# Optimization experiments

Measured on AMD Instinct MI355X. Metric: run time of the kernel, lower is better.

Reference implementation:

```python
import jax, jax.numpy as jnp
import numpy as np

EMBED_DIM = 1024
N_HEADS = 16
HEAD_DIM = EMBED_DIM // N_HEADS


def setup_inputs() -> dict:
    key = jax.random.key(0)
    ks = jax.random.split(key, 11)
    B, S = 4, 2048
    s = 0.02
    return {
        "queries": jax.random.normal(ks[0], (B, S, EMBED_DIM), dtype=jnp.float32),
        "keys": jax.random.normal(ks[1], (B, S, EMBED_DIM), dtype=jnp.float32),
        "values": jax.random.normal(ks[2], (B, S, EMBED_DIM), dtype=jnp.float32),
        "W_q": jax.random.normal(ks[3], (HEAD_DIM, HEAD_DIM), dtype=jnp.float32) * s,
        "b_q": jax.random.normal(ks[4], (HEAD_DIM,), dtype=jnp.float32) * s,
        "W_k": jax.random.normal(ks[5], (HEAD_DIM, HEAD_DIM), dtype=jnp.float32) * s,
        "b_k": jax.random.normal(ks[6], (HEAD_DIM,), dtype=jnp.float32) * s,
        "W_v": jax.random.normal(ks[7], (HEAD_DIM, HEAD_DIM), dtype=jnp.float32) * s,
        "b_v": jax.random.normal(ks[8], (HEAD_DIM,), dtype=jnp.float32) * s,
        "W_p": jax.random.normal(ks[9], (EMBED_DIM, EMBED_DIM), dtype=jnp.float32) * s,
        "b_p": jax.random.normal(ks[10], (EMBED_DIM,), dtype=jnp.float32) * s,
    }


def reference(queries, keys, values, W_q, b_q, W_k, b_k, W_v, b_v, W_p, b_p):
    B, S, _ = queries.shape
    scale = HEAD_DIM ** 0.5  # module uses head_dim ** (1/2)
    # split heads: [B, S, H, hd]
    q = queries.reshape(B, S, N_HEADS, HEAD_DIM)
    k = keys.reshape(B, S, N_HEADS, HEAD_DIM)
    v = values.reshape(B, S, N_HEADS, HEAD_DIM)
    # per-head projections (weights shared across heads); torch Linear: x @ W.T + b
    q = jnp.einsum('bshd,ed->bhse', q, W_q) + b_q
    k = jnp.einsum('bshd,ed->bhse', k, W_k) + b_k
    v = jnp.einsum('bshd,ed->bhse', v, W_v) + b_v
    # scaled dot-product attention
    scores = jnp.einsum('bhqd,bhkd->bhqk', q, k) / scale  # [B,H,S,S]
    attn = jax.nn.softmax(scores, axis=-1)
    ctx = jnp.einsum('bhqk,bhkd->bhqd', attn, v)  # [B,H,S,hd]
    # merge heads and final projection
    ctx = ctx.transpose(0, 2, 1, 3).reshape(B, S, EMBED_DIM)
    return ctx @ W_p.T + b_p
```

## Files before the change

### kernel.cpp

```cpp
#include <hip/hip_runtime.h>
#include <hip/hip_bf16.h>

#define EMBED 1024
#define NH 16
#define HD 64
#define BSZ 4
#define SSZ 2048
#define LSTR 72

typedef __attribute__((ext_vector_type(8))) short short8;
typedef __attribute__((ext_vector_type(4))) short short4v;
typedef __attribute__((ext_vector_type(4))) float float4v;
typedef __attribute__((ext_vector_type(2))) unsigned int uint2v;

__device__ inline float4v mfma16(short8 a, short8 b, float4v c) {
    return __builtin_amdgcn_mfma_f32_16x16x32_bf16(a, b, c, 0, 0, 0);
}

__device__ inline float fexp2(float x) { return __builtin_amdgcn_exp2f(x); }

__device__ inline short f2bf(float f) {
    unsigned u = __builtin_bit_cast(unsigned, f);
    return (short)((u + 0x8000u) >> 16);
}
__device__ inline unsigned pk2(float a, float b) {
    unsigned ua = __builtin_bit_cast(unsigned, a);
    unsigned ub = __builtin_bit_cast(unsigned, b);
    return ((ua + 0x8000u) >> 16) | (((ub + 0x8000u) >> 16) << 16);
}
__device__ inline short8 ld8_f32_bf16(const float* p) {
    float4v lo = *(const float4v*)p;
    float4v hi = *(const float4v*)(p + 4);
    short8 r;
#pragma unroll
    for (int i = 0; i < 4; ++i) { r[i] = f2bf(lo[i]); r[i + 4] = f2bf(hi[i]); }
    return r;
}

__device__ inline void glds16(const short* gsrc, short* ldst) {
    __builtin_amdgcn_global_load_lds(
        (const __attribute__((address_space(1))) unsigned int*)gsrc,
        (__attribute__((address_space(3))) unsigned int*)ldst,
        16, 0, 0);
}

__global__ __launch_bounds__(256) void wp_cvt_kernel(
    const float* __restrict__ Wp, short* __restrict__ Wpb)
{
    int i = (blockIdx.x * 256 + threadIdx.x) * 4;
    float4v v = *(const float4v*)(Wp + i);
    short4v s;
#pragma unroll
    for (int j = 0; j < 4; ++j) s[j] = f2bf(v[j]);
    *(short4v*)(Wpb + i) = s;
}

__global__ __launch_bounds__(256) void qkv_kernel(
    const float* __restrict__ q_in, const float* __restrict__ k_in,
    const float* __restrict__ v_in,
    const float* __restrict__ Wq, const float* __restrict__ bq,
    const float* __restrict__ Wk, const float* __restrict__ bk,
    const float* __restrict__ Wv, const float* __restrict__ bv,
    short* __restrict__ qp, short* __restrict__ kp, short* __restrict__ vt)
{
    __shared__ __align__(16) short Xb[64 * LSTR];
    __shared__ __align__(16) short Wb[64 * LSTR];

    int z = blockIdx.z;
    const float* X    = z == 0 ? q_in : (z == 1 ? k_in : v_in);
    const float* W    = z == 0 ? Wq   : (z == 1 ? Wk   : Wv);
    const float* bias = z == 0 ? bq   : (z == 1 ? bk   : bv);
    const float scale = z == 0 ? 0.125f * 1.44269504f : 1.0f;

    int tid = threadIdx.x;
    int wave = tid >> 6, lane = tid & 63, quad = lane >> 4, l16 = lane & 15;
    int h = blockIdx.y;
    int rbase = blockIdx.x * 64;
    int b = rbase >> 11;
    int sbase = rbase & (SSZ - 1);
    int bh = b * NH + h;

    int srow = tid >> 2, c16 = (tid & 3) * 16;
    {
        const float* xsrc = X + (size_t)(rbase + srow) * EMBED + h * HD + c16;
        short8 x0 = ld8_f32_bf16(xsrc);
        short8 x1 = ld8_f32_bf16(xsrc + 8);
        *(short8*)&Xb[srow * LSTR + c16] = x0;
        *(short8*)&Xb[srow * LSTR + c16 + 8] = x1;
        const float* wsrc = W + (size_t)srow * HD + c16;
        short8 w0 = ld8_f32_bf16(wsrc);
        short8 w1 = ld8_f32_bf16(wsrc + 8);
        *(short8*)&Wb[srow * LSTR + c16] = w0;
        *(short8*)&Wb[srow * LSTR + c16 + 8] = w1;
    }
    __syncthreads();

    short8 a0 = *(const short8*)&Xb[(wave * 16 + l16) * LSTR + quad * 8];
    short8 a1 = *(const short8*)&Xb[(wave * 16 + l16) * LSTR + 32 + quad * 8];
    float4v acc[4];
#pragma unroll
    for (int nt = 0; nt < 4; ++nt) acc[nt] = (float4v)(0.f);
#pragma unroll
    for (int nt = 0; nt < 4; ++nt) {
        short8 b0 = *(const short8*)&Wb[(nt * 16 + l16) * LSTR + quad * 8];
        short8 b1 = *(const short8*)&Wb[(nt * 16 + l16) * LSTR + 32 + quad * 8];
        acc[nt] = mfma16(a0, b0, acc[nt]);
        acc[nt] = mfma16(a1, b1, acc[nt]);
    }
    __syncthreads();

    if (z < 2) {
#pragma unroll
        for (int nt = 0; nt < 4; ++nt) {
            float bv_ = bias[nt * 16 + l16];
#pragma unroll
            for (int r = 0; r < 4; ++r) {
                float val = (acc[nt][r] + bv_) * scale;
                Xb[(wave * 16 + quad * 4 + r) * LSTR + nt * 16 + l16] = f2bf(val);
            }
        }
        __syncthreads();
        short8 r0 = *(const short8*)&Xb[srow * LSTR + c16];
        short8 r1 = *(const short8*)&Xb[srow * LSTR + c16 + 8];
        short* Y = z == 0 ? qp : kp;
        size_t o = ((size_t)bh * SSZ + sbase + srow) * HD + c16;
        *(short8*)&Y[o] = r0;
        *(short8*)&Y[o + 8] = r1;
    } else {
#pragma unroll
        for (int nt = 0; nt < 4; ++nt) {
            float bv_ = bias[nt * 16 + l16];
            uint2v p;
            p[0] = pk2(acc[nt][0] + bv_, acc[nt][1] + bv_);
            p[1] = pk2(acc[nt][2] + bv_, acc[nt][3] + bv_);
            *(uint2v*)&Xb[(nt * 16 + l16) * LSTR + wave * 16 + quad * 4] = p;
        }
        __syncthreads();
        short8 r0 = *(const short8*)&Xb[srow * LSTR + c16];
        short8 r1 = *(const short8*)&Xb[srow * LSTR + c16 + 8];
        size_t o = ((size_t)bh * HD + srow) * SSZ + sbase + c16;
        *(short8*)&vt[o] = r0;
        *(short8*)&vt[o + 8] = r1;
    }
}

__global__ __launch_bounds__(512, 4) void attn_kernel(
    const short* __restrict__ qp, const short* __restrict__ kp,
    const short* __restrict__ vt, short* __restrict__ ctx)
{
    __shared__ __align__(16) short Kls[64 * LSTR];
    __shared__ __align__(16) short Vls[64 * LSTR];
    __shared__ __align__(16) short Pl[8 * 32 * LSTR];

    int tid = threadIdx.x;
    int wave = tid >> 6, lane = tid & 63, quad = lane >> 4, l16 = lane & 15;
    int bh = blockIdx.x;
    int b = bh >> 4, h = bh & 15;
    int qrow0 = blockIdx.y * 256 + wave * 32;

    const short* Qb = qp + (size_t)bh * SSZ * HD;
    const short* Kb = kp + (size_t)bh * SSZ * HD;
    const short* Vb = vt + (size_t)bh * HD * SSZ;

    int srow = tid >> 3;
    int scol = (tid & 7) * 8;
    const short* ksrc = Kb + srow * HD + scol;
    const short* vsrc = Vb + (size_t)srow * SSZ + scol;
    short* kdst = &Kls[srow * LSTR + scol];
    short* vdst = &Vls[srow * LSTR + scol];

    short8 qf[2][2];
#pragma unroll
    for (int nt = 0; nt < 2; ++nt)
#pragma unroll
        for (int c = 0; c < 2; ++c)
            qf[nt][c] = *(const short8*)&Qb[(size_t)(qrow0 + nt * 16 + l16) * HD + c * 32 + quad * 8];

    const short one = (short)0x3F80;
    short8 ones = {one, one, one, one, one, one, one, one};

    float4v oacc[4][2];
#pragma unroll
    for (int dt = 0; dt < 4; ++dt)
#pragma unroll
        for (int nt = 0; nt < 2; ++nt) oacc[dt][nt] = (float4v)(0.f);
    float4v lacc[2];
    lacc[0] = (float4v)(0.f); lacc[1] = (float4v)(0.f);

    short* Pw = Pl + wave * 32 * LSTR;

    {
        short8 kr = *(const short8*)(ksrc);
        short8 vr = *(const short8*)(vsrc);
        *(short8*)kdst = kr;
        *(short8*)vdst = vr;
    }
    __syncthreads();

    for (int kt = 0; kt < SSZ / 64; ++kt) {
        short8 krn, vrn;
        if (kt < 31) {
            krn = *(const short8*)(ksrc + (kt + 1) * 64 * HD);
            vrn = *(const short8*)(vsrc + (kt + 1) * 64);
        }
        float4v sacc[4][2];
#pragma unroll
        for (int mt = 0; mt < 4; ++mt) {
            sacc[mt][0] = (float4v)(0.f); sacc[mt][1] = (float4v)(0.f);
        }
#pragma unroll
        for (int mt = 0; mt < 4; ++mt)
#pragma unroll
            for (int c = 0; c < 2; ++c) {
                short8 kf = *(const short8*)&Kls[(mt * 16 + l16) * LSTR + c * 32 + quad * 8];
                sacc[mt][0] = mfma16(kf, qf[0][c], sacc[mt][0]);
                sacc[mt][1] = mfma16(kf, qf[1][c], sacc[mt][1]);
            }
#pragma unroll
        for (int mt = 0; mt < 4; ++mt)
#pragma unroll
            for (int nt = 0; nt < 2; ++nt) {
                float e0 = fexp2(sacc[mt][nt][0]);
                float e1 = fexp2(sacc[mt][nt][1]);
                float e2 = fexp2(sacc[mt][nt][2]);
                float e3 = fexp2(sacc[mt][nt][3]);
                uint2v p; p[0] = pk2(e0, e1); p[1] = pk2(e2, e3);
                *(uint2v*)&Pw[(nt * 16 + l16) * LSTR + mt * 16 + quad * 4] = p;
            }
        short8 pf[2][2];
#pragma unroll
        for (int nt = 0; nt < 2; ++nt)
#pragma unroll
            for (int c = 0; c < 2; ++c)
                pf[nt][c] = *(const short8*)&Pw[(nt * 16 + l16) * LSTR + c * 32 + quad * 8];
#pragma unroll
        for (int nt = 0; nt < 2; ++nt)
#pragma unroll
            for (int c = 0; c < 2; ++c)
                lacc[nt] = mfma16(ones, pf[nt][c], lacc[nt]);
#pragma unroll
        for (int dt = 0; dt < 4; ++dt)
#pragma unroll
            for (int c = 0; c < 2; ++c) {
                short8 vf = *(const short8*)&Vls[(dt * 16 + l16) * LSTR + c * 32 + quad * 8];
                oacc[dt][0] = mfma16(vf, pf[0][c], oacc[dt][0]);
                oacc[dt][1] = mfma16(vf, pf[1][c], oacc[dt][1]);
            }
        __syncthreads();
        if (kt < 31) {
            *(short8*)kdst = krn;
            *(short8*)vdst = vrn;
        }
        __syncthreads();
    }
    float rl[2];
    rl[0] = 1.0f / lacc[0][0];
    rl[1] = 1.0f / lacc[1][0];
#pragma unroll
    for (int dt = 0; dt < 4; ++dt)
#pragma unroll
        for (int nt = 0; nt < 2; ++nt) {
            uint2v p;
            p[0] = pk2(oacc[dt][nt][0] * rl[nt], oacc[dt][nt][1] * rl[nt]);
            p[1] = pk2(oacc[dt][nt][2] * rl[nt], oacc[dt][nt][3] * rl[nt]);
            size_t o = ((size_t)(b * SSZ + qrow0 + nt * 16 + l16)) * EMBED
                       + h * HD + dt * 16 + quad * 4;
            *(uint2v*)&ctx[o] = p;
        }
}

__global__ __launch_bounds__(256) void proj_kernel(
    const short* __restrict__ ctx, const short* __restrict__ Wpb,
    const float* __restrict__ bp, float* __restrict__ out)
{
    __shared__ __align__(16) short Als[128 * 64];
    __shared__ __align__(16) short Bls[128 * 64];

    int tid = threadIdx.x;
    int wave = tid >> 6, lane = tid & 63, quad = lane >> 4, l16 = lane & 15;
    int wm = wave >> 1, wn = wave & 1;
    int row0 = blockIdx.x * 128;
    int col0 = blockIdx.y * 128;

    int lrow = lane >> 3;
    int lcol = (lane & 7) * 8;
    const short* ag = ctx + (size_t)(row0 + wave * 32 + lrow) * EMBED + lcol;
    const short* bg = Wpb + (size_t)(col0 + wave * 32 + lrow) * EMBED + lcol;

    float4v acc[4][4];
#pragma unroll
    for (int mt = 0; mt < 4; ++mt)
#pragma unroll
        for (int nt = 0; nt < 4; ++nt) acc[mt][nt] = (float4v)(0.f);

    for (int kc = 0; kc < EMBED / 64; ++kc) {
#pragma unroll
        for (int i = 0; i < 4; ++i) {
            glds16(ag + (size_t)(i * 8) * EMBED + kc * 64,
                   &Als[(wave * 32 + i * 8) * 64]);
            glds16(bg + (size_t)(i * 8) * EMBED + kc * 64,
                   &Bls[(wave * 32 + i * 8) * 64]);
        }
        __syncthreads();
#pragma unroll
        for (int ks = 0; ks < 2; ++ks) {
            short8 af[4], bf[4];
#pragma unroll
            for (int mt = 0; mt < 4; ++mt)
                af[mt] = *(const short8*)&Als[(wm * 64 + mt * 16 + l16) * 64 + ks * 32 + quad * 8];
#pragma unroll
            for (int nt = 0; nt < 4; ++nt)
                bf[nt] = *(const short8*)&Bls[(wn * 64 + nt * 16 + l16) * 64 + ks * 32 + quad * 8];
#pragma unroll
            for (int mt = 0; mt < 4; ++mt)
#pragma unroll
                for (int nt = 0; nt < 4; ++nt)
                    acc[mt][nt] = mfma16(af[mt], bf[nt], acc[mt][nt]);
        }
        __syncthreads();
    }
#pragma unroll
    for (int nt = 0; nt < 4; ++nt) {
        float bias = bp[col0 + wn * 64 + nt * 16 + l16];
#pragma unroll
        for (int mt = 0; mt < 4; ++mt)
#pragma unroll
            for (int r = 0; r < 4; ++r) {
                int row = row0 + wm * 64 + mt * 16 + quad * 4 + r;
                out[(size_t)row * EMBED + col0 + wn * 64 + nt * 16 + l16] = acc[mt][nt][r] + bias;
            }
    }
}

extern "C" void kernel_launch(void* const* d_in, const int* in_sizes, int n_in,
                              void* d_out, int out_size, void* d_ws, size_t ws_size,
                              hipStream_t stream) {
    const float* q_in = (const float*)d_in[0];
    const float* k_in = (const float*)d_in[1];
    const float* v_in = (const float*)d_in[2];
    const float* Wq   = (const float*)d_in[3];
    const float* bq   = (const float*)d_in[4];
    const float* Wk   = (const float*)d_in[5];
    const float* bk   = (const float*)d_in[6];
    const float* Wv   = (const float*)d_in[7];
    const float* bv   = (const float*)d_in[8];
    const float* Wp   = (const float*)d_in[9];
    const float* bp   = (const float*)d_in[10];

    const size_t TENS = (size_t)BSZ * SSZ * EMBED;
    short* ws  = (short*)d_ws;
    short* qp  = ws;
    short* kp  = qp + TENS;
    short* vtp = kp + TENS;
    short* ctx = vtp + TENS;
    short* wpb = ctx + TENS;

    wp_cvt_kernel<<<dim3(EMBED * EMBED / 1024), 256, 0, stream>>>(Wp, wpb);
    qkv_kernel<<<dim3(BSZ * SSZ / 64, NH, 3), 256, 0, stream>>>(
        q_in, k_in, v_in, Wq, bq, Wk, bk, Wv, bv, qp, kp, vtp);
    attn_kernel<<<dim3(BSZ * NH, SSZ / 256), 512, 0, stream>>>(qp, kp, vtp, ctx);
    proj_kernel<<<dim3(BSZ * SSZ / 128, EMBED / 128), 256, 0, stream>>>(
        ctx, wpb, bp, (float*)d_out);
}
```

Measured before the change: 277.6 us.

## Restructure QKV projection: 16-row blocks over all heads, register-resident weights

The QKV projection kernel now gives each block 16 sequence rows and all 16 heads, with each wave handling 4 heads. Shared weight fragments are loaded once into registers and reused across heads, cutting the 3D grid to 2D and removing the LDS staging of X. For Q/K the MFMA operands are swapped so results are written straight to global memory. V goes through a small per-wave LDS buffer for the transpose, and the bf16 packing now uses a byte-permute intrinsic. The trade-off is smaller, less coalesced global writes, with more work and more registers per block.

Measured after the change: 282.7 us. About the same (+1.8%).

```diff
diff --git a/kernel.cpp b/kernel.cpp
--- a/kernel.cpp
+++ b/kernel.cpp
@@ -7,11 +7,12 @@
 #define BSZ 4
 #define SSZ 2048
 #define LSTR 72
+#define BSTR 24
 
 typedef __attribute__((ext_vector_type(8))) short short8;
-typedef __attribute__((ext_vector_type(4))) short short4v;
 typedef __attribute__((ext_vector_type(4))) float float4v;
 typedef __attribute__((ext_vector_type(2))) unsigned int uint2v;
+typedef __attribute__((ext_vector_type(4))) unsigned int uint4v;
 
 __device__ inline float4v mfma16(short8 a, short8 b, float4v c) {
     return __builtin_amdgcn_mfma_f32_16x16x32_bf16(a, b, c, 0, 0, 0);
@@ -19,22 +20,19 @@
 
 __device__ inline float fexp2(float x) { return __builtin_amdgcn_exp2f(x); }
 
-__device__ inline short f2bf(float f) {
-    unsigned u = __builtin_bit_cast(unsigned, f);
-    return (short)((u + 0x8000u) >> 16);
-}
 __device__ inline unsigned pk2(float a, float b) {
-    unsigned ua = __builtin_bit_cast(unsigned, a);
-    unsigned ub = __builtin_bit_cast(unsigned, b);
-    return ((ua + 0x8000u) >> 16) | (((ub + 0x8000u) >> 16) << 16);
-}
+    unsigned ua = __builtin_bit_cast(unsigned, a) + 0x8000u;
+    unsigned ub = __builtin_bit_cast(unsigned, b) + 0x8000u;
+    return __builtin_amdgcn_perm(ub, ua, 0x07060302u);
+}
+
 __device__ inline short8 ld8_f32_bf16(const float* p) {
     float4v lo = *(const float4v*)p;
     float4v hi = *(const float4v*)(p + 4);
-    short8 r;
-#pragma unroll
-    for (int i = 0; i < 4; ++i) { r[i] = f2bf(lo[i]); r[i + 4] = f2bf(hi[i]); }
-    return r;
+    uint4v u;
+    u[0] = pk2(lo[0], lo[1]); u[1] = pk2(lo[2], lo[3]);
+    u[2] = pk2(hi[0], hi[1]); u[3] = pk2(hi[2], hi[3]);
+    return __builtin_bit_cast(short8, u);
 }
 
 __device__ inline void glds16(const short* gsrc, short* ldst) {
@@ -49,10 +47,10 @@
 {
     int i = (blockIdx.x * 256 + threadIdx.x) * 4;
     float4v v = *(const float4v*)(Wp + i);
-    short4v s;
-#pragma unroll
-    for (int j = 0; j < 4; ++j) s[j] = f2bf(v[j]);
-    *(short4v*)(Wpb + i) = s;
+    uint2v s;
+    s[0] = pk2(v[0], v[1]);
+    s[1] = pk2(v[2], v[3]);
+    *(uint2v*)(Wpb + i) = s;
 }
 
 __global__ __launch_bounds__(256) void qkv_kernel(
@@ -63,10 +61,10 @@
     const float* __restrict__ Wv, const float* __restrict__ bv,
     short* __restrict__ qp, short* __restrict__ kp, short* __restrict__ vt)
 {
-    __shared__ __align__(16) short Xb[64 * LSTR];
     __shared__ __align__(16) short Wb[64 * LSTR];
-
-    int z = blockIdx.z;
+    __shared__ __align__(16) short Bnc[4][64 * BSTR];
+
+    int z = blockIdx.y;
     const float* X    = z == 0 ? q_in : (z == 1 ? k_in : v_in);
     const float* W    = z == 0 ? Wq   : (z == 1 ? Wk   : Wv);
     const float* bias = z == 0 ? bq   : (z == 1 ? bk   : bv);
@@ -74,73 +72,92 @@
 
     int tid = threadIdx.x;
     int wave = tid >> 6, lane = tid & 63, quad = lane >> 4, l16 = lane & 15;
-    int h = blockIdx.y;
-    int rbase = blockIdx.x * 64;
+    int rbase = blockIdx.x * 16;
     int b = rbase >> 11;
     int sbase = rbase & (SSZ - 1);
-    int bh = b * NH + h;
-
-    int srow = tid >> 2, c16 = (tid & 3) * 16;
+
     {
-        const float* xsrc = X + (size_t)(rbase + srow) * EMBED + h * HD + c16;
-        short8 x0 = ld8_f32_bf16(xsrc);
-        short8 x1 = ld8_f32_bf16(xsrc + 8);
-        *(short8*)&Xb[srow * LSTR + c16] = x0;
-        *(short8*)&Xb[srow * LSTR + c16 + 8] = x1;
-        const float* wsrc = W + (size_t)srow * HD + c16;
-        short8 w0 = ld8_f32_bf16(wsrc);
-        short8 w1 = ld8_f32_bf16(wsrc + 8);
-        *(short8*)&Wb[srow * LSTR + c16] = w0;
-        *(short8*)&Wb[srow * LSTR + c16 + 8] = w1;
+        int wrow = tid >> 2, wc16 = (tid & 3) * 16;
+        const float* wsrc = W + wrow * HD + wc16;
+        *(short8*)&Wb[wrow * LSTR + wc16]     = ld8_f32_bf16(wsrc);
+        *(short8*)&Wb[wrow * LSTR + wc16 + 8] = ld8_f32_bf16(wsrc + 8);
     }
     __syncthreads();
 
-    short8 a0 = *(const short8*)&Xb[(wave * 16 + l16) * LSTR + quad * 8];
-    short8 a1 = *(const short8*)&Xb[(wave * 16 + l16) * LSTR + 32 + quad * 8];
-    float4v acc[4];
-#pragma unroll
-    for (int nt = 0; nt < 4; ++nt) acc[nt] = (float4v)(0.f);
-#pragma unroll
-    for (int nt = 0; nt < 4; ++nt) {
-        short8 b0 = *(const short8*)&Wb[(nt * 16 + l16) * LSTR + quad * 8];
-        short8 b1 = *(const short8*)&Wb[(nt * 16 + l16) * LSTR + 32 + quad * 8];
-        acc[nt] = mfma16(a0, b0, acc[nt]);
-        acc[nt] = mfma16(a1, b1, acc[nt]);
-    }
-    __syncthreads();
+    short8 wf[4][2];
+#pragma unroll
+    for (int t = 0; t < 4; ++t)
+#pragma unroll
+        for (int c = 0; c < 2; ++c)
+            wf[t][c] = *(const short8*)&Wb[(t * 16 + l16) * LSTR + c * 32 + quad * 8];
+
+    const float* xrow = X + (size_t)(rbase + l16) * EMBED;
 
     if (z < 2) {
-#pragma unroll
-        for (int nt = 0; nt < 4; ++nt) {
-            float bv_ = bias[nt * 16 + l16];
-#pragma unroll
-            for (int r = 0; r < 4; ++r) {
-                float val = (acc[nt][r] + bv_) * scale;
-                Xb[(wave * 16 + quad * 4 + r) * LSTR + nt * 16 + l16] = f2bf(val);
-            }
-        }
-        __syncthreads();
-        short8 r0 = *(const short8*)&Xb[srow * LSTR + c16];
-        short8 r1 = *(const short8*)&Xb[srow * LSTR + c16 + 8];
         short* Y = z == 0 ? qp : kp;
-        size_t o = ((size_t)bh * SSZ + sbase + srow) * HD + c16;
-        *(short8*)&Y[o] = r0;
-        *(short8*)&Y[o + 8] = r1;
+        float4v bv4[4];
+#pragma unroll
+        for (int dt = 0; dt < 4; ++dt)
+            bv4[dt] = *(const float4v*)&bias[dt * 16 + quad * 4];
+#pragma unroll
+        for (int hh = 0; hh < 4; ++hh) {
+            int h = wave * 4 + hh;
+            const float* xs = xrow + h * HD + quad * 8;
+            short8 xf0 = ld8_f32_bf16(xs);
+            short8 xf1 = ld8_f32_bf16(xs + 32);
+            float4v acc[4];
+#pragma unroll
+            for (int dt = 0; dt < 4; ++dt) acc[dt] = (float4v)(0.f);
+#pragma unroll
+            for (int dt = 0; dt < 4; ++dt) {
+                acc[dt] = mfma16(wf[dt][0], xf0, acc[dt]);
+                acc[dt] = mfma16(wf[dt][1], xf1, acc[dt]);
+            }
+            size_t ybase = ((size_t)(b * NH + h) * SSZ + sbase + l16) * HD;
+#pragma unroll
+            for (int dt = 0; dt < 4; ++dt) {
+                float t0 = (acc[dt][0] + bv4[dt][0]) * scale;
+                float t1 = (acc[dt][1] + bv4[dt][1]) * scale;
+                float t2 = (acc[dt][2] + bv4[dt][2]) * scale;
+                float t3 = (acc[dt][3] + bv4[dt][3]) * scale;
+                uint2v p; p[0] = pk2(t0, t1); p[1] = pk2(t2, t3);
+                *(uint2v*)&Y[ybase + dt * 16 + quad * 4] = p;
+            }
+        }
     } else {
-#pragma unroll
-        for (int nt = 0; nt < 4; ++nt) {
-            float bv_ = bias[nt * 16 + l16];
-            uint2v p;
-            p[0] = pk2(acc[nt][0] + bv_, acc[nt][1] + bv_);
-            p[1] = pk2(acc[nt][2] + bv_, acc[nt][3] + bv_);
-            *(uint2v*)&Xb[(nt * 16 + l16) * LSTR + wave * 16 + quad * 4] = p;
-        }
-        __syncthreads();
-        short8 r0 = *(const short8*)&Xb[srow * LSTR + c16];
-        short8 r1 = *(const short8*)&Xb[srow * LSTR + c16 + 8];
-        size_t o = ((size_t)bh * HD + srow) * SSZ + sbase + c16;
-        *(short8*)&vt[o] = r0;
-        *(short8*)&vt[o + 8] = r1;
+        short* bw = &Bnc[wave][0];
+        float bvs[4];
+#pragma unroll
+        for (int nt = 0; nt < 4; ++nt) bvs[nt] = bias[nt * 16 + l16];
+#pragma unroll
+        for (int hh = 0; hh < 4; ++hh) {
+            int h = wave * 4 + hh;
+            const float* xs = xrow + h * HD + quad * 8;
+            short8 xf0 = ld8_f32_bf16(xs);
+            short8 xf1 = ld8_f32_bf16(xs + 32);
+            float4v acc[4];
+#pragma unroll
+            for (int nt = 0; nt < 4; ++nt) acc[nt] = (float4v)(0.f);
+#pragma unroll
+            for (int nt = 0; nt < 4; ++nt) {
+                acc[nt] = mfma16(xf0, wf[nt][0], acc[nt]);
+                acc[nt] = mfma16(xf1, wf[nt][1], acc[nt]);
+            }
+#pragma unroll
+            for (int nt = 0; nt < 4; ++nt) {
+                float t0 = acc[nt][0] + bvs[nt];
+                float t1 = acc[nt][1] + bvs[nt];
+                float t2 = acc[nt][2] + bvs[nt];
+                float t3 = acc[nt][3] + bvs[nt];
+                uint2v p; p[0] = pk2(t0, t1); p[1] = pk2(t2, t3);
+                *(uint2v*)&bw[(nt * 16 + l16) * BSTR + quad * 4] = p;
+            }
+            short8 v0 = *(const short8*)&bw[lane * BSTR];
+            short8 v1 = *(const short8*)&bw[lane * BSTR + 8];
+            size_t o = ((size_t)(b * NH + h) * HD + lane) * SSZ + sbase;
+            *(short8*)&vt[o] = v0;
+            *(short8*)&vt[o + 8] = v1;
+        }
     }
 }
 
@@ -356,7 +373,7 @@
     short* wpb = ctx + TENS;
 
     wp_cvt_kernel<<<dim3(EMBED * EMBED / 1024), 256, 0, stream>>>(Wp, wpb);
-    qkv_kernel<<<dim3(BSZ * SSZ / 64, NH, 3), 256, 0, stream>>>(
+    qkv_kernel<<<dim3(BSZ * SSZ / 16, 3), 256, 0, stream>>>(
         q_in, k_in, v_in, Wq, bq, Wk, bk, Wv, bv, qp, kp, vtp);
     attn_kernel<<<dim3(BSZ * NH, SSZ / 256), 512, 0, stream>>>(qp, kp, vtp, ctx);
     proj_kernel<<<dim3(BSZ * SSZ / 128, EMBED / 128), 256, 0, stream>>>(
```
